# Performance work log

Measured on AMD Instinct MI355X. Metric: run time of the kernel, lower is better.

The kernel has to match this reference:

```python
import jax, jax.numpy as jnp
import numpy as np

NUM_HEADS = 8
KEY_DIM = 16
BLOCK = 8
HALO = 3
KV_K = BLOCK + 2 * HALO          # kv_kernel = 14
EMB = NUM_HEADS * KEY_DIM        # 128


def setup_inputs() -> dict:
    key = jax.random.key(0)
    ks = jax.random.split(key, 6)
    B, H, W, C = 8, 80, 80, 128
    std = KEY_DIM ** -0.5
    return {
        "inputs": jax.random.normal(ks[0], (B, H, W, C), jnp.float32),
        "query_dense": jax.random.normal(ks[1], (C, EMB), jnp.float32) * 0.05,
        "kv_dense": jax.random.normal(ks[2], (C, 2 * EMB), jnp.float32) * 0.05,
        "out_dense": jax.random.normal(ks[3], (EMB, C), jnp.float32) * 0.05,
        "pos_emb_w": jax.random.normal(ks[4], (KEY_DIM, 2 * KV_K - 1), jnp.float32) * std,
        "pos_emb_h": jax.random.normal(ks[5], (KEY_DIM, 2 * KV_K - 1), jnp.float32) * std,
    }


def rel_to_abs(rel_pos):
    # [b, heads, hh, ww, 2*pos_dim-1] -> [b, heads, hh, ww, pos_dim]
    b, heads, hh, ww, dim = rel_pos.shape
    pos_dim = (dim + 1) // 2
    gap = pos_dim - ww if ww > 1 else 2
    flat = rel_pos.reshape(b, heads, hh, ww * dim)
    flat = flat[:, :, :, ww - 1:-1] if ww > 1 else flat[:, :, :, 1:]
    out = flat.reshape(b, heads, hh, ww, 2 * (pos_dim - 1))
    return out[..., gap:pos_dim + gap]


def relative_logits(pos_q, pe_w, pe_h):
    # pos_q: [b, n, qb, qb, key_dim]
    rl_w = rel_to_abs(jnp.einsum('bnxyd,dk->bnxyk', pos_q, pe_w))                       # [b,n,qb,qb,KV_K]
    qh = pos_q.transpose(0, 1, 3, 2, 4)
    rl_h = rel_to_abs(jnp.einsum('bnxyd,dk->bnxyk', qh, pe_h)).transpose(0, 1, 3, 2, 4)  # [b,n,qb,qb,KV_K]
    return rl_w[..., None, :] + rl_h[..., :, None]                                       # [b,n,qb,qb,KV_K,KV_K]


def reference(inputs, query_dense, kv_dense, out_dense, pos_emb_w, pos_emb_h):
    B, H, W, C = inputs.shape
    scale = 1.0 / jnp.sqrt(jnp.asarray(KEY_DIM, inputs.dtype))
    query = jnp.einsum('bhwc,cd->bhwd', inputs, query_dense) * scale
    hq, wq = H // BLOCK, W // BLOCK
    q = query.reshape(B, hq, BLOCK, wq, BLOCK, NUM_HEADS, KEY_DIM).transpose(0, 5, 1, 3, 2, 4, 6)
    attn_q = q.reshape(B, NUM_HEADS, hq, wq, BLOCK * BLOCK, KEY_DIM)
    pos_q = q.reshape(B, NUM_HEADS * hq * wq, BLOCK, BLOCK, KEY_DIM)

    kv = jnp.einsum('bhwc,cd->bhwd', inputs, kv_dense)
    kvp = jnp.pad(kv, ((0, 0), (HALO, HALO), (HALO, HALO), (0, 0)))
    # overlapping halo windows: stride BLOCK, window KV_K (matches tf.image.extract_patches)
    ridx = jnp.arange(hq)[:, None] * BLOCK + jnp.arange(KV_K)[None, :]
    cidx = jnp.arange(wq)[:, None] * BLOCK + jnp.arange(KV_K)[None, :]
    patches = kvp[:, ridx][:, :, :, cidx]                 # [B,hq,KV,wq,KV,2*EMB]
    patches = patches.transpose(0, 1, 3, 2, 4, 5)         # [B,hq,wq,KV,KV,2*EMB]
    kv_inp = patches.reshape(B, hq, wq, KV_K, KV_K, NUM_HEADS, 2 * KEY_DIM)
    kv_inp = kv_inp.transpose(0, 5, 1, 2, 3, 4, 6).reshape(B, NUM_HEADS, hq, wq, KV_K * KV_K, 2 * KEY_DIM)
    k, v = kv_inp[..., :KEY_DIM], kv_inp[..., KEY_DIM:]

    scores = jnp.einsum('bnhwqd,bnhwkd->bnhwqk', attn_q, k)   # [B,heads,hq,wq,64,196]
    pos = relative_logits(pos_q, pos_emb_w, pos_emb_h)
    scores = scores + pos.reshape(scores.shape)
    attn = jax.nn.softmax(scores, axis=-1)
    out = jnp.einsum('bnhwqk,bnhwkd->bnhwqd', attn, v)
    out = out.reshape(B, NUM_HEADS, hq, wq, BLOCK, BLOCK, KEY_DIM)
    out = out.transpose(0, 2, 4, 3, 5, 1, 6).reshape(B, H, W, EMB)
    return jnp.einsum('bhwe,eo->bhwo', out, out_dense)
```

## Files before the change

### kernel.cpp

```cpp
#include <hip/hip_runtime.h>
#include <cstddef>

namespace {
constexpr int BATCH = 8;
constexpr int HDIM  = 80;
constexpr int WDIM  = 80;
constexpr int CDIM  = 128;
constexpr int NH    = 8;
constexpr int KD    = 16;
constexpr int BLK   = 8;
constexpr int HALO  = 3;
constexpr int KVK   = 14;
constexpr int EMB   = 128;
constexpr int HQ    = 10;
constexpr int WQ    = 10;
constexpr int MROWS = BATCH * HDIM * WDIM;
constexpr int QKV_N = 384;

constexpr int KPAD  = 24;
constexpr int M2PAD = 36;
constexpr int PEPAD = 20;
constexpr int APAD  = 136;
}

typedef _Float16 f16;
typedef f16   f16x2 __attribute__((ext_vector_type(2)));
typedef f16   f16x4 __attribute__((ext_vector_type(4)));
typedef f16   f16x8 __attribute__((ext_vector_type(8)));
typedef float f32x4 __attribute__((ext_vector_type(4)));

__global__ __launch_bounds__(256) void convert_weights(
    const float* __restrict__ qd, const float* __restrict__ kvd,
    const float* __restrict__ od, const float* __restrict__ pew,
    const float* __restrict__ peh,
    f16* __restrict__ BTqkv, f16* __restrict__ BTo, f16* __restrict__ peT)
{
  const float QSC = 0.25f * 1.4426950408889634f;
  int tid = blockIdx.x * 256 + threadIdx.x;
  if (tid < 384 * 128) {
    int n = tid >> 7, c = tid & 127;
    float v = (n < 128) ? qd[c * 128 + n] * QSC : kvd[c * 256 + (n - 128)];
    BTqkv[tid] = (f16)v;
  } else if (tid < 384 * 128 + 128 * 128) {
    int j = tid - 384 * 128;
    int o = j >> 7, e = j & 127;
    BTo[j] = (f16)od[e * 128 + o];
  } else {
    int j = tid - (384 * 128 + 128 * 128);
    int which = j / 640;
    int rem   = j - which * 640;
    int col   = rem / PEPAD;
    int d     = rem - col * PEPAD;
    float v = 0.f;
    if (col < 27 && d < 16) v = (which ? peh : pew)[d * 27 + col];
    peT[j] = (f16)v;
  }
}

__global__ __launch_bounds__(256, 4) void gemm_qkv_mfma(
    const float* __restrict__ A, const f16* __restrict__ BT,
    f16* __restrict__ C)
{
  __shared__ __align__(16) f16 b_lds[128 * APAD];

  const int bid = blockIdx.x;
  const int xcd = bid & 7;
  const int idx = bid >> 3;
  const int m0 = (xcd * 50 + idx / 3) * 128;
  const int n0 = (idx % 3) * 128;
  const int t  = threadIdx.x;

  #pragma unroll
  for (int it = 0; it < 8; ++it) {
    int item = t + it * 256;
    int row = item >> 4, c8 = item & 15;
    *reinterpret_cast<f16x8*>(&b_lds[row * APAD + c8 * 8]) =
        *reinterpret_cast<const f16x8*>(BT + (size_t)(n0 + row) * CDIM + c8 * 8);
  }
  __syncthreads();

  const int lane = t & 63, wv = t >> 6;
  const int g = lane >> 4, qi = lane & 15;

  const float* ap0 = A + (size_t)(m0 + wv * 32 + qi) * CDIM + g * 4;
  const float* ap1 = ap0 + 16 * CDIM;

  f32x4 acc[2][8];
  #pragma unroll
  for (int mt = 0; mt < 2; ++mt)
    #pragma unroll
    for (int nt = 0; nt < 8; ++nt) acc[mt][nt] = {0.f, 0.f, 0.f, 0.f};

  #pragma unroll
  for (int ks = 0; ks < 8; ++ks) {
    float4 fa0 = *reinterpret_cast<const float4*>(ap0 + ks * 16);
    float4 fa1 = *reinterpret_cast<const float4*>(ap1 + ks * 16);
    f16x4 a0 = {(f16)fa0.x, (f16)fa0.y, (f16)fa0.z, (f16)fa0.w};
    f16x4 a1 = {(f16)fa1.x, (f16)fa1.y, (f16)fa1.z, (f16)fa1.w};
    #pragma unroll
    for (int nt = 0; nt < 8; ++nt) {
      f16x4 bf = *reinterpret_cast<const f16x4*>(
          &b_lds[(nt * 16 + qi) * APAD + ks * 16 + g * 4]);
      acc[0][nt] = __builtin_amdgcn_mfma_f32_16x16x16f16(bf, a0, acc[0][nt], 0, 0, 0);
      acc[1][nt] = __builtin_amdgcn_mfma_f32_16x16x16f16(bf, a1, acc[1][nt], 0, 0, 0);
    }
  }

  #pragma unroll
  for (int mt = 0; mt < 2; ++mt) {
    int m = m0 + wv * 32 + mt * 16 + qi;
    #pragma unroll
    for (int nt = 0; nt < 8; ++nt) {
      f16x4 h = {(f16)acc[mt][nt][0], (f16)acc[mt][nt][1],
                 (f16)acc[mt][nt][2], (f16)acc[mt][nt][3]};
      *reinterpret_cast<f16x4*>(&C[(size_t)m * QKV_N + n0 + nt * 16 + g * 4]) = h;
    }
  }
}

__global__ __launch_bounds__(256, 4) void halo_attn_mfma(
    const f16* __restrict__ qkv, const f16* __restrict__ peT,
    f16* __restrict__ O)
{
  __shared__ __align__(16) f16 k_lds[224 * KPAD];
  __shared__ __align__(16) f16 v_lds[224 * 16];
  __shared__ __align__(16) f16 m2_lds[64 * M2PAD];

  const int d0w  = blockIdx.x;
  const int bid  = (d0w & 7) * 800 + (d0w >> 3);
  const int n    = bid & 7;
  const int tile = bid >> 3;
  const int tw   = tile % WQ;
  const int th   = (tile / WQ) % HQ;
  const int b    = tile / (WQ * HQ);
  const int t    = threadIdx.x;

  const int lane = t & 63;
  const int wv   = t >> 6;
  const int g    = lane >> 4;
  const int qi   = lane & 15;
  const int q0   = wv * 16;
  const int q    = q0 + qi;
  const int x    = q >> 3, y = q & 7;

  const size_t qrow = ((size_t)(b * HDIM + th * BLK + x)) * WDIM + tw * BLK + y;
  f16x4 qf = *reinterpret_cast<const f16x4*>(&qkv[qrow * QKV_N + n * KD + g * 4]);

  #pragma unroll
  for (int it = 0; it < 4; ++it) {
    int item = t + it * 256;
    if (item < 896) {
      int slot = item >> 2, part = item & 3;
      int kh = slot >> 4, kw = slot & 15;
      int hh = th * BLK - HALO + kh;
      int ww = tw * BLK - HALO + kw;
      f16x8 v = {};
      if ((unsigned)hh < (unsigned)HDIM && (unsigned)ww < (unsigned)WDIM) {
        size_t row = ((size_t)(b * HDIM + hh)) * WDIM + ww;
        v = *reinterpret_cast<const f16x8*>(
            &qkv[row * QKV_N + 128 + n * 32 + part * 8]);
      }
      if (part < 2)
        *reinterpret_cast<f16x8*>(&k_lds[slot * KPAD + part * 8]) = v;
      else
        *reinterpret_cast<f16x8*>(&v_lds[slot * 16 + (part - 2) * 8]) = v;
    }
  }

  const f32x4 z4 = {0.f, 0.f, 0.f, 0.f};

  #pragma unroll
  for (int which = 0; which < 2; ++which) {
    #pragma unroll
    for (int ct = 0; ct < 2; ++ct) {
      f16x4 pf = *reinterpret_cast<const f16x4*>(
          &peT[(which * 32 + ct * 16 + qi) * PEPAD + g * 4]);
      f32x4 mc = __builtin_amdgcn_mfma_f32_16x16x16f16(qf, pf, z4, 0, 0, 0);
      int colb = ct * 16 + qi;
      #pragma unroll
      for (int r = 0; r < 4; ++r) {
        int qr = q0 + g * 4 + r;
        if (which == 0) {
          int kw = colb - 13 + (qr & 7);
          if ((unsigned)kw < 16u) m2_lds[qr * M2PAD + kw] = (f16)mc[r];
        } else {
          int tt = colb - 13 + (qr >> 3);
          if ((unsigned)tt < 14u) m2_lds[qr * M2PAD + 16 + tt] = (f16)mc[r];
        }
      }
    }
  }

  f16x4 rlwv = *reinterpret_cast<const f16x4*>(&m2_lds[q * M2PAD + g * 4]);
  f16x4 rh4[4];
  #pragma unroll
  for (int k = 0; k < 4; ++k)
    rh4[k] = *reinterpret_cast<const f16x4*>(&m2_lds[q * M2PAD + 16 + k * 4]);

  float rlw[4];
  #pragma unroll
  for (int r = 0; r < 4; ++r) rlw[r] = (float)rlwv[r];
  if (g == 3) { rlw[2] = -1e30f; rlw[3] = -1e30f; }

  __syncthreads();

  f32x4 s[14];
  #pragma unroll
  for (int tt = 0; tt < 14; ++tt) {
    float rh = (float)rh4[tt >> 2][tt & 3];
    f32x4 c;
    c[0] = rlw[0] + rh; c[1] = rlw[1] + rh;
    c[2] = rlw[2] + rh; c[3] = rlw[3] + rh;
    f16x4 kf = *reinterpret_cast<const f16x4*>(&k_lds[(tt * 16 + qi) * KPAD + g * 4]);
    s[tt] = __builtin_amdgcn_mfma_f32_16x16x16f16(kf, qf, c, 0, 0, 0);
  }

  float ls = 0.f;
  f16x4 pf[14];
  #pragma unroll
  for (int tt = 0; tt < 14; ++tt) {
    float p0 = __builtin_amdgcn_exp2f(s[tt][0]);
    float p1 = __builtin_amdgcn_exp2f(s[tt][1]);
    float p2 = __builtin_amdgcn_exp2f(s[tt][2]);
    float p3 = __builtin_amdgcn_exp2f(s[tt][3]);
    ls += (p0 + p1) + (p2 + p3);
    f16x2 lo = __builtin_bit_cast(f16x2, __builtin_amdgcn_cvt_pkrtz(p0, p1));
    f16x2 hi = __builtin_bit_cast(f16x2, __builtin_amdgcn_cvt_pkrtz(p2, p3));
    pf[tt][0] = lo[0]; pf[tt][1] = lo[1];
    pf[tt][2] = hi[0]; pf[tt][3] = hi[1];
  }
  ls += __shfl_xor(ls, 16);
  ls += __shfl_xor(ls, 32);

  f16x4 iv;
  #pragma unroll
  for (int r = 0; r < 4; ++r)
    iv[r] = (qi == g * 4 + r) ? (f16)1.f : (f16)0.f;

  f32x4 acc = z4;
  #pragma unroll
  for (int tt = 0; tt < 14; ++tt) {
    f16x4 xv = *reinterpret_cast<const f16x4*>(&v_lds[(tt * 16 + qi) * 16 + g * 4]);
    f32x4 tD = __builtin_amdgcn_mfma_f32_16x16x16f16(xv, iv, z4, 0, 0, 0);
    f16x2 lo = __builtin_bit_cast(f16x2, __builtin_amdgcn_cvt_pkrtz(tD[0], tD[1]));
    f16x2 hi = __builtin_bit_cast(f16x2, __builtin_amdgcn_cvt_pkrtz(tD[2], tD[3]));
    f16x4 vf;
    vf[0] = lo[0]; vf[1] = lo[1]; vf[2] = hi[0]; vf[3] = hi[1];
    acc = __builtin_amdgcn_mfma_f32_16x16x16f16(vf, pf[tt], acc, 0, 0, 0);
  }

  const float inv = __builtin_amdgcn_rcpf(ls);
  f16x4 o = {(f16)(acc[0] * inv), (f16)(acc[1] * inv),
             (f16)(acc[2] * inv), (f16)(acc[3] * inv)};
  *reinterpret_cast<f16x4*>(&O[qrow * EMB + n * KD + g * 4]) = o;
}

__global__ __launch_bounds__(256, 4) void gemm_out_mfma(
    const f16* __restrict__ A, const f16* __restrict__ BT,
    float* __restrict__ C)
{
  __shared__ __align__(16) f16 b_lds[128 * APAD];

  const int m0 = blockIdx.x * 64;
  const int t  = threadIdx.x;

  #pragma unroll
  for (int it = 0; it < 8; ++it) {
    int item = t + it * 256;
    int row = item >> 4, c8 = item & 15;
    *reinterpret_cast<f16x8*>(&b_lds[row * APAD + c8 * 8]) =
        *reinterpret_cast<const f16x8*>(BT + (size_t)row * EMB + c8 * 8);
  }
  __syncthreads();

  const int lane = t & 63, wv = t >> 6;
  const int g = lane >> 4, qi = lane & 15;

  const f16* ap = A + (size_t)(m0 + wv * 16 + qi) * EMB + g * 4;

  f32x4 acc[8];
  #pragma unroll
  for (int nt = 0; nt < 8; ++nt) acc[nt] = {0.f, 0.f, 0.f, 0.f};

  #pragma unroll
  for (int ks = 0; ks < 8; ++ks) {
    f16x4 a = *reinterpret_cast<const f16x4*>(ap + ks * 16);
    #pragma unroll
    for (int nt = 0; nt < 8; ++nt) {
      f16x4 bf = *reinterpret_cast<const f16x4*>(
          &b_lds[(nt * 16 + qi) * APAD + ks * 16 + g * 4]);
      acc[nt] = __builtin_amdgcn_mfma_f32_16x16x16f16(bf, a, acc[nt], 0, 0, 0);
    }
  }

  const int m = m0 + wv * 16 + qi;
  #pragma unroll
  for (int nt = 0; nt < 8; ++nt) {
    f32x4 v = acc[nt];
    *reinterpret_cast<float4*>(&C[(size_t)m * CDIM + nt * 16 + g * 4]) =
        *reinterpret_cast<float4*>(&v);
  }
}

extern "C" void kernel_launch(void* const* d_in, const int* in_sizes, int n_in,
                              void* d_out, int out_size, void* d_ws, size_t ws_size,
                              hipStream_t stream)
{
  const float* inputs = (const float*)d_in[0];
  const float* qd     = (const float*)d_in[1];
  const float* kvd    = (const float*)d_in[2];
  const float* od     = (const float*)d_in[3];
  const float* pew    = (const float*)d_in[4];
  const float* peh    = (const float*)d_in[5];

  char* ws = (char*)d_ws;
  f16* qkv   = (f16*)ws;
  f16* O     = (f16*)(ws + (size_t)MROWS * QKV_N * 2);
  f16* BTqkv = (f16*)(ws + (size_t)MROWS * QKV_N * 2 + (size_t)MROWS * EMB * 2);
  f16* BTo   = BTqkv + 384 * 128;
  f16* peT   = BTo + 128 * 128;
  float* out = (float*)d_out;

  convert_weights<<<dim3(261), 256, 0, stream>>>(qd, kvd, od, pew, peh,
                                                 BTqkv, BTo, peT);
  gemm_qkv_mfma<<<dim3(1200), 256, 0, stream>>>(inputs, BTqkv, qkv);
  halo_attn_mfma<<<dim3(BATCH * HQ * WQ * NH), 256, 0, stream>>>(qkv, peT, O);
  gemm_out_mfma<<<dim3(MROWS / 64), 256, 0, stream>>>(O, BTo, out);
}
```

Baseline: 73.25 us.

## Store K/V in per-head zero-padded spatial layout for branch-free halo loads

The QKV GEMM now writes Q to its own buffer and scatters K/V into a per-(batch, head) spatially padded buffer (86x88x32). A new kernel zeroes the 3-pixel halo border. The attention kernel then loads halo windows without bounds checks, and each head's 64-byte K/V row sits contiguously with its neighbours. In exchange there is an extra small launch, and the GEMM epilogue does more scattered stores with index math.

```diff
diff --git a/kernel.cpp b/kernel.cpp
--- a/kernel.cpp
+++ b/kernel.cpp
@@ -16,6 +16,11 @@
 constexpr int WQ    = 10;
 constexpr int MROWS = BATCH * HDIM * WDIM;
 constexpr int QKV_N = 384;
+
+constexpr int PH    = 86;
+constexpr int PW    = 88;
+constexpr int KVCH  = 32;
+constexpr int HEADSZ = PH * PW * KVCH;
 
 constexpr int KPAD  = 24;
 constexpr int M2PAD = 36;
@@ -57,9 +62,28 @@
   }
 }
 
+__global__ __launch_bounds__(256) void zero_pad(f16* __restrict__ kvp)
+{
+  f16* base = kvp + (size_t)blockIdx.x * HEADSZ;
+  for (int item = threadIdx.x; item < 1168 * 4; item += 256) {
+    int cell = item >> 2, part = item & 3;
+    int hh, ww;
+    if (cell < 6 * PW) {
+      int r = cell / PW; ww = cell - r * PW;
+      hh = (r < 3) ? r : 80 + r;
+    } else {
+      int c = cell - 6 * PW;
+      int r = c >> 3, cc = c & 7;
+      hh = 3 + r;
+      ww = (cc < 3) ? cc : 80 + cc;
+    }
+    *reinterpret_cast<f16x8*>(base + (hh * PW + ww) * KVCH + part * 8) = f16x8{};
+  }
+}
+
 __global__ __launch_bounds__(256, 4) void gemm_qkv_mfma(
     const float* __restrict__ A, const f16* __restrict__ BT,
-    f16* __restrict__ C)
+    f16* __restrict__ Qbuf, f16* __restrict__ kvp)
 {
   __shared__ __align__(16) f16 b_lds[128 * APAD];
 
@@ -109,18 +133,34 @@
   #pragma unroll
   for (int mt = 0; mt < 2; ++mt) {
     int m = m0 + wv * 32 + mt * 16 + qi;
-    #pragma unroll
-    for (int nt = 0; nt < 8; ++nt) {
-      f16x4 h = {(f16)acc[mt][nt][0], (f16)acc[mt][nt][1],
-                 (f16)acc[mt][nt][2], (f16)acc[mt][nt][3]};
-      *reinterpret_cast<f16x4*>(&C[(size_t)m * QKV_N + n0 + nt * 16 + g * 4]) = h;
+    if (n0 == 0) {
+      #pragma unroll
+      for (int nt = 0; nt < 8; ++nt) {
+        f16x4 h = {(f16)acc[mt][nt][0], (f16)acc[mt][nt][1],
+                   (f16)acc[mt][nt][2], (f16)acc[mt][nt][3]};
+        *reinterpret_cast<f16x4*>(&Qbuf[(size_t)m * EMB + nt * 16 + g * 4]) = h;
+      }
+    } else {
+      int bb  = m / 6400;
+      int rem = m - bb * 6400;
+      int hh  = rem / 80;
+      int ww  = rem - hh * 80;
+      size_t pbase = (size_t)bb * (NH * HEADSZ) + ((hh + 3) * PW + (ww + 3)) * KVCH;
+      #pragma unroll
+      for (int nt = 0; nt < 8; ++nt) {
+        int col  = (n0 - 128) + nt * 16 + g * 4;
+        int head = col >> 5, cc = col & 31;
+        f16x4 h = {(f16)acc[mt][nt][0], (f16)acc[mt][nt][1],
+                   (f16)acc[mt][nt][2], (f16)acc[mt][nt][3]};
+        *reinterpret_cast<f16x4*>(&kvp[pbase + (size_t)head * HEADSZ + cc]) = h;
+      }
     }
   }
 }
 
 __global__ __launch_bounds__(256, 4) void halo_attn_mfma(
-    const f16* __restrict__ qkv, const f16* __restrict__ peT,
-    f16* __restrict__ O)
+    const f16* __restrict__ Qbuf, const f16* __restrict__ kvp,
+    const f16* __restrict__ peT, f16* __restrict__ O)
 {
   __shared__ __align__(16) f16 k_lds[224 * KPAD];
   __shared__ __align__(16) f16 v_lds[224 * 16];
@@ -144,22 +184,18 @@
   const int x    = q >> 3, y = q & 7;
 
   const size_t qrow = ((size_t)(b * HDIM + th * BLK + x)) * WDIM + tw * BLK + y;
-  f16x4 qf = *reinterpret_cast<const f16x4*>(&qkv[qrow * QKV_N + n * KD + g * 4]);
-
+  f16x4 qf = *reinterpret_cast<const f16x4*>(&Qbuf[qrow * EMB + n * KD + g * 4]);
+
+  const f16* kvbase = kvp + (size_t)(b * NH + n) * HEADSZ
+                    + ((th * BLK) * PW + tw * BLK) * KVCH;
   #pragma unroll
   for (int it = 0; it < 4; ++it) {
     int item = t + it * 256;
     if (item < 896) {
       int slot = item >> 2, part = item & 3;
       int kh = slot >> 4, kw = slot & 15;
-      int hh = th * BLK - HALO + kh;
-      int ww = tw * BLK - HALO + kw;
-      f16x8 v = {};
-      if ((unsigned)hh < (unsigned)HDIM && (unsigned)ww < (unsigned)WDIM) {
-        size_t row = ((size_t)(b * HDIM + hh)) * WDIM + ww;
-        v = *reinterpret_cast<const f16x8*>(
-            &qkv[row * QKV_N + 128 + n * 32 + part * 8]);
-      }
+      f16x8 v = *reinterpret_cast<const f16x8*>(
+          kvbase + kh * (PW * KVCH) + kw * KVCH + part * 8);
       if (part < 2)
         *reinterpret_cast<f16x8*>(&k_lds[slot * KPAD + part * 8]) = v;
       else
@@ -313,17 +349,18 @@
   const float* pew    = (const float*)d_in[4];
   const float* peh    = (const float*)d_in[5];
 
-  char* ws = (char*)d_ws;
-  f16* qkv   = (f16*)ws;
-  f16* O     = (f16*)(ws + (size_t)MROWS * QKV_N * 2);
-  f16* BTqkv = (f16*)(ws + (size_t)MROWS * QKV_N * 2 + (size_t)MROWS * EMB * 2);
+  f16* Qbuf  = (f16*)d_ws;
+  f16* kvp   = Qbuf + (size_t)MROWS * EMB;
+  f16* O     = kvp + (size_t)BATCH * NH * HEADSZ;
+  f16* BTqkv = O + (size_t)MROWS * EMB;
   f16* BTo   = BTqkv + 384 * 128;
   f16* peT   = BTo + 128 * 128;
   float* out = (float*)d_out;
 
   convert_weights<<<dim3(261), 256, 0, stream>>>(qd, kvd, od, pew, peh,
                                                  BTqkv, BTo, peT);
-  gemm_qkv_mfma<<<dim3(1200), 256, 0, stream>>>(inputs, BTqkv, qkv);
-  halo_attn_mfma<<<dim3(BATCH * HQ * WQ * NH), 256, 0, stream>>>(qkv, peT, O);
+  zero_pad<<<dim3(BATCH * NH), 256, 0, stream>>>(kvp);
+  gemm_qkv_mfma<<<dim3(1200), 256, 0, stream>>>(inputs, BTqkv, Qbuf, kvp);
+  halo_attn_mfma<<<dim3(BATCH * HQ * WQ * NH), 256, 0, stream>>>(Qbuf, kvp, peT, O);
   gemm_out_mfma<<<dim3(MROWS / 64), 256, 0, stream>>>(O, BTo, out);
 }
```

Result: no change. 74.63 us (+1.9%).

## Fuse output projection into halo attention kernel, looping heads per block

Applied to the files above, without the earlier changes.

The attention kernel now processes all 8 heads of a spatial tile inside one block, accumulating each head's output times the matching slice of the output projection into per-thread fp32 accumulators. It then writes the final fp32 output directly, which removes the separate output GEMM launch and the f16 intermediate O buffer round trip. In exchange the grid shrinks from 6400 to 800 blocks, each running a serial head loop with extra barriers. The projection weights are read from global memory instead of LDS, and launch bounds drop to 3 blocks per SM to make room for the added accumulator registers.

```diff
diff --git a/kernel.cpp b/kernel.cpp
--- a/kernel.cpp
+++ b/kernel.cpp
@@ -118,21 +118,19 @@
   }
 }
 
-__global__ __launch_bounds__(256, 4) void halo_attn_mfma(
+__global__ __launch_bounds__(256, 3) void halo_attn_fused(
     const f16* __restrict__ qkv, const f16* __restrict__ peT,
-    f16* __restrict__ O)
+    const f16* __restrict__ BTo, float* __restrict__ out)
 {
   __shared__ __align__(16) f16 k_lds[224 * KPAD];
   __shared__ __align__(16) f16 v_lds[224 * 16];
   __shared__ __align__(16) f16 m2_lds[64 * M2PAD];
 
   const int d0w  = blockIdx.x;
-  const int bid  = (d0w & 7) * 800 + (d0w >> 3);
-  const int n    = bid & 7;
-  const int tile = bid >> 3;
-  const int tw   = tile % WQ;
-  const int th   = (tile / WQ) % HQ;
-  const int b    = tile / (WQ * HQ);
+  const int bid  = (d0w & 7) * 100 + (d0w >> 3);
+  const int tw   = bid % WQ;
+  const int th   = (bid / WQ) % HQ;
+  const int b    = bid / (WQ * HQ);
   const int t    = threadIdx.x;
 
   const int lane = t & 63;
@@ -144,160 +142,134 @@
   const int x    = q >> 3, y = q & 7;
 
   const size_t qrow = ((size_t)(b * HDIM + th * BLK + x)) * WDIM + tw * BLK + y;
-  f16x4 qf = *reinterpret_cast<const f16x4*>(&qkv[qrow * QKV_N + n * KD + g * 4]);
-
-  #pragma unroll
-  for (int it = 0; it < 4; ++it) {
-    int item = t + it * 256;
-    if (item < 896) {
-      int slot = item >> 2, part = item & 3;
-      int kh = slot >> 4, kw = slot & 15;
-      int hh = th * BLK - HALO + kh;
-      int ww = tw * BLK - HALO + kw;
-      f16x8 v = {};
-      if ((unsigned)hh < (unsigned)HDIM && (unsigned)ww < (unsigned)WDIM) {
-        size_t row = ((size_t)(b * HDIM + hh)) * WDIM + ww;
-        v = *reinterpret_cast<const f16x8*>(
-            &qkv[row * QKV_N + 128 + n * 32 + part * 8]);
+  const f32x4 z4 = {0.f, 0.f, 0.f, 0.f};
+
+  f32x4 out_acc[8];
+  #pragma unroll
+  for (int nt = 0; nt < 8; ++nt) out_acc[nt] = z4;
+
+  for (int n = 0; n < NH; ++n) {
+    __syncthreads();
+
+    f16x4 qf = *reinterpret_cast<const f16x4*>(&qkv[qrow * QKV_N + n * KD + g * 4]);
+
+    #pragma unroll
+    for (int it = 0; it < 4; ++it) {
+      int item = t + it * 256;
+      if (item < 896) {
+        int slot = item >> 2, part = item & 3;
+        int kh = slot >> 4, kw = slot & 15;
+        int hh = th * BLK - HALO + kh;
+        int ww = tw * BLK - HALO + kw;
+        f16x8 v = {};
+        if ((unsigned)hh < (unsigned)HDIM && (unsigned)ww < (unsigned)WDIM) {
+          size_t row = ((size_t)(b * HDIM + hh)) * WDIM + ww;
+          v = *reinterpret_cast<const f16x8*>(
+              &qkv[row * QKV_N + 128 + n * 32 + part * 8]);
+        }
+        if (part < 2)
+          *reinterpret_cast<f16x8*>(&k_lds[slot * KPAD + part * 8]) = v;
+        else
+          *reinterpret_cast<f16x8*>(&v_lds[slot * 16 + (part - 2) * 8]) = v;
       }
-      if (part < 2)
-        *reinterpret_cast<f16x8*>(&k_lds[slot * KPAD + part * 8]) = v;
-      else
-        *reinterpret_cast<f16x8*>(&v_lds[slot * 16 + (part - 2) * 8]) = v;
-    }
-  }
-
-  const f32x4 z4 = {0.f, 0.f, 0.f, 0.f};
-
-  #pragma unroll
-  for (int which = 0; which < 2; ++which) {
-    #pragma unroll
-    for (int ct = 0; ct < 2; ++ct) {
-      f16x4 pf = *reinterpret_cast<const f16x4*>(
-          &peT[(which * 32 + ct * 16 + qi) * PEPAD + g * 4]);
-      f32x4 mc = __builtin_amdgcn_mfma_f32_16x16x16f16(qf, pf, z4, 0, 0, 0);
-      int colb = ct * 16 + qi;
+    }
+
+    #pragma unroll
+    for (int which = 0; which < 2; ++which) {
       #pragma unroll
-      for (int r = 0; r < 4; ++r) {
-        int qr = q0 + g * 4 + r;
-        if (which == 0) {
-          int kw = colb - 13 + (qr & 7);
-          if ((unsigned)kw < 16u) m2_lds[qr * M2PAD + kw] = (f16)mc[r];
-        } else {
-          int tt = colb - 13 + (qr >> 3);
-          if ((unsigned)tt < 14u) m2_lds[qr * M2PAD + 16 + tt] = (f16)mc[r];
+      for (int ct = 0; ct < 2; ++ct) {
+        f16x4 pf = *reinterpret_cast<const f16x4*>(
+            &peT[(which * 32 + ct * 16 + qi) * PEPAD + g * 4]);
+        f32x4 mc = __builtin_amdgcn_mfma_f32_16x16x16f16(qf, pf, z4, 0, 0, 0);
+        int colb = ct * 16 + qi;
+        #pragma unroll
+        for (int r = 0; r < 4; ++r) {
+          int qr = q0 + g * 4 + r;
+          if (which == 0) {
+            int kw = colb - 13 + (qr & 7);
+            if ((unsigned)kw < 16u) m2_lds[qr * M2PAD + kw] = (f16)mc[r];
+          } else {
+            int tt = colb - 13 + (qr >> 3);
+            if ((unsigned)tt < 14u) m2_lds[qr * M2PAD + 16 + tt] = (f16)mc[r];
+          }
         }
       }
     }
-  }
-
-  f16x4 rlwv = *reinterpret_cast<const f16x4*>(&m2_lds[q * M2PAD + g * 4]);
-  f16x4 rh4[4];
-  #pragma unroll
-  for (int k = 0; k < 4; ++k)
-    rh4[k] = *reinterpret_cast<const f16x4*>(&m2_lds[q * M2PAD + 16 + k * 4]);
-
-  float rlw[4];
-  #pragma unroll
-  for (int r = 0; r < 4; ++r) rlw[r] = (float)rlwv[r];
-  if (g == 3) { rlw[2] = -1e30f; rlw[3] = -1e30f; }
-
-  __syncthreads();
-
-  f32x4 s[14];
-  #pragma unroll
-  for (int tt = 0; tt < 14; ++tt) {
-    float rh = (float)rh4[tt >> 2][tt & 3];
-    f32x4 c;
-    c[0] = rlw[0] + rh; c[1] = rlw[1] + rh;
-    c[2] = rlw[2] + rh; c[3] = rlw[3] + rh;
-    f16x4 kf = *reinterpret_cast<const f16x4*>(&k_lds[(tt * 16 + qi) * KPAD + g * 4]);
-    s[tt] = __builtin_amdgcn_mfma_f32_16x16x16f16(kf, qf, c, 0, 0, 0);
-  }
-
-  float ls = 0.f;
-  f16x4 pf[14];
-  #pragma unroll
-  for (int tt = 0; tt < 14; ++tt) {
-    float p0 = __builtin_amdgcn_exp2f(s[tt][0]);
-    float p1 = __builtin_amdgcn_exp2f(s[tt][1]);
-    float p2 = __builtin_amdgcn_exp2f(s[tt][2]);
-    float p3 = __builtin_amdgcn_exp2f(s[tt][3]);
-    ls += (p0 + p1) + (p2 + p3);
-    f16x2 lo = __builtin_bit_cast(f16x2, __builtin_amdgcn_cvt_pkrtz(p0, p1));
-    f16x2 hi = __builtin_bit_cast(f16x2, __builtin_amdgcn_cvt_pkrtz(p2, p3));
-    pf[tt][0] = lo[0]; pf[tt][1] = lo[1];
-    pf[tt][2] = hi[0]; pf[tt][3] = hi[1];
-  }
-  ls += __shfl_xor(ls, 16);
-  ls += __shfl_xor(ls, 32);
-
-  f16x4 iv;
-  #pragma unroll
-  for (int r = 0; r < 4; ++r)
-    iv[r] = (qi == g * 4 + r) ? (f16)1.f : (f16)0.f;
-
-  f32x4 acc = z4;
-  #pragma unroll
-  for (int tt = 0; tt < 14; ++tt) {
-    f16x4 xv = *reinterpret_cast<const f16x4*>(&v_lds[(tt * 16 + qi) * 16 + g * 4]);
-    f32x4 tD = __builtin_amdgcn_mfma_f32_16x16x16f16(xv, iv, z4, 0, 0, 0);
-    f16x2 lo = __builtin_bit_cast(f16x2, __builtin_amdgcn_cvt_pkrtz(tD[0], tD[1]));
-    f16x2 hi = __builtin_bit_cast(f16x2, __builtin_amdgcn_cvt_pkrtz(tD[2], tD[3]));
-    f16x4 vf;
-    vf[0] = lo[0]; vf[1] = lo[1]; vf[2] = hi[0]; vf[3] = hi[1];
-    acc = __builtin_amdgcn_mfma_f32_16x16x16f16(vf, pf[tt], acc, 0, 0, 0);
-  }
-
-  const float inv = __builtin_amdgcn_rcpf(ls);
-  f16x4 o = {(f16)(acc[0] * inv), (f16)(acc[1] * inv),
-             (f16)(acc[2] * inv), (f16)(acc[3] * inv)};
-  *reinterpret_cast<f16x4*>(&O[qrow * EMB + n * KD + g * 4]) = o;
-}
-
-__global__ __launch_bounds__(256, 4) void gemm_out_mfma(
-    const f16* __restrict__ A, const f16* __restrict__ BT,
-    float* __restrict__ C)
-{
-  __shared__ __align__(16) f16 b_lds[128 * APAD];
-
-  const int m0 = blockIdx.x * 64;
-  const int t  = threadIdx.x;
-
-  #pragma unroll
-  for (int it = 0; it < 8; ++it) {
-    int item = t + it * 256;
-    int row = item >> 4, c8 = item & 15;
-    *reinterpret_cast<f16x8*>(&b_lds[row * APAD + c8 * 8]) =
-        *reinterpret_cast<const f16x8*>(BT + (size_t)row * EMB + c8 * 8);
-  }
-  __syncthreads();
-
-  const int lane = t & 63, wv = t >> 6;
-  const int g = lane >> 4, qi = lane & 15;
-
-  const f16* ap = A + (size_t)(m0 + wv * 16 + qi) * EMB + g * 4;
-
-  f32x4 acc[8];
-  #pragma unroll
-  for (int nt = 0; nt < 8; ++nt) acc[nt] = {0.f, 0.f, 0.f, 0.f};
-
-  #pragma unroll
-  for (int ks = 0; ks < 8; ++ks) {
-    f16x4 a = *reinterpret_cast<const f16x4*>(ap + ks * 16);
+
+    f16x4 rlwv = *reinterpret_cast<const f16x4*>(&m2_lds[q * M2PAD + g * 4]);
+    f16x4 rh4[4];
+    #pragma unroll
+    for (int k = 0; k < 4; ++k)
+      rh4[k] = *reinterpret_cast<const f16x4*>(&m2_lds[q * M2PAD + 16 + k * 4]);
+
+    float rlw[4];
+    #pragma unroll
+    for (int r = 0; r < 4; ++r) rlw[r] = (float)rlwv[r];
+    if (g == 3) { rlw[2] = -1e30f; rlw[3] = -1e30f; }
+
+    __syncthreads();
+
+    f32x4 s[14];
+    #pragma unroll
+    for (int tt = 0; tt < 14; ++tt) {
+      float rh = (float)rh4[tt >> 2][tt & 3];
+      f32x4 c;
+      c[0] = rlw[0] + rh; c[1] = rlw[1] + rh;
+      c[2] = rlw[2] + rh; c[3] = rlw[3] + rh;
+      f16x4 kf = *reinterpret_cast<const f16x4*>(&k_lds[(tt * 16 + qi) * KPAD + g * 4]);
+      s[tt] = __builtin_amdgcn_mfma_f32_16x16x16f16(kf, qf, c, 0, 0, 0);
+    }
+
+    float ls = 0.f;
+    f16x4 pf[14];
+    #pragma unroll
+    for (int tt = 0; tt < 14; ++tt) {
+      float p0 = __builtin_amdgcn_exp2f(s[tt][0]);
+      float p1 = __builtin_amdgcn_exp2f(s[tt][1]);
+      float p2 = __builtin_amdgcn_exp2f(s[tt][2]);
+      float p3 = __builtin_amdgcn_exp2f(s[tt][3]);
+      ls += (p0 + p1) + (p2 + p3);
+      f16x2 lo = __builtin_bit_cast(f16x2, __builtin_amdgcn_cvt_pkrtz(p0, p1));
+      f16x2 hi = __builtin_bit_cast(f16x2, __builtin_amdgcn_cvt_pkrtz(p2, p3));
+      pf[tt][0] = lo[0]; pf[tt][1] = lo[1];
+      pf[tt][2] = hi[0]; pf[tt][3] = hi[1];
+    }
+    ls += __shfl_xor(ls, 16);
+    ls += __shfl_xor(ls, 32);
+
+    f16x4 iv;
+    #pragma unroll
+    for (int r = 0; r < 4; ++r)
+      iv[r] = (qi == g * 4 + r) ? (f16)1.f : (f16)0.f;
+
+    f32x4 acc = z4;
+    #pragma unroll
+    for (int tt = 0; tt < 14; ++tt) {
+      f16x4 xv = *reinterpret_cast<const f16x4*>(&v_lds[(tt * 16 + qi) * 16 + g * 4]);
+      f32x4 tD = __builtin_amdgcn_mfma_f32_16x16x16f16(xv, iv, z4, 0, 0, 0);
+      f16x2 lo = __builtin_bit_cast(f16x2, __builtin_amdgcn_cvt_pkrtz(tD[0], tD[1]));
+      f16x2 hi = __builtin_bit_cast(f16x2, __builtin_amdgcn_cvt_pkrtz(tD[2], tD[3]));
+      f16x4 vf;
+      vf[0] = lo[0]; vf[1] = lo[1]; vf[2] = hi[0]; vf[3] = hi[1];
+      acc = __builtin_amdgcn_mfma_f32_16x16x16f16(vf, pf[tt], acc, 0, 0, 0);
+    }
+
+    const float inv = __builtin_amdgcn_rcpf(ls);
+    f16x4 of = {(f16)(acc[0] * inv), (f16)(acc[1] * inv),
+                (f16)(acc[2] * inv), (f16)(acc[3] * inv)};
+
     #pragma unroll
     for (int nt = 0; nt < 8; ++nt) {
       f16x4 bf = *reinterpret_cast<const f16x4*>(
-          &b_lds[(nt * 16 + qi) * APAD + ks * 16 + g * 4]);
-      acc[nt] = __builtin_amdgcn_mfma_f32_16x16x16f16(bf, a, acc[nt], 0, 0, 0);
-    }
-  }
-
-  const int m = m0 + wv * 16 + qi;
+          &BTo[(size_t)(nt * 16 + qi) * EMB + n * KD + g * 4]);
+      out_acc[nt] = __builtin_amdgcn_mfma_f32_16x16x16f16(bf, of, out_acc[nt], 0, 0, 0);
+    }
+  }
+
   #pragma unroll
   for (int nt = 0; nt < 8; ++nt) {
-    f32x4 v = acc[nt];
-    *reinterpret_cast<float4*>(&C[(size_t)m * CDIM + nt * 16 + g * 4]) =
+    f32x4 v = out_acc[nt];
+    *reinterpret_cast<float4*>(&out[qrow * EMB + nt * 16 + g * 4]) =
         *reinterpret_cast<float4*>(&v);
   }
 }
@@ -315,8 +287,7 @@
 
   char* ws = (char*)d_ws;
   f16* qkv   = (f16*)ws;
-  f16* O     = (f16*)(ws + (size_t)MROWS * QKV_N * 2);
-  f16* BTqkv = (f16*)(ws + (size_t)MROWS * QKV_N * 2 + (size_t)MROWS * EMB * 2);
+  f16* BTqkv = (f16*)(ws + (size_t)MROWS * QKV_N * 2);
   f16* BTo   = BTqkv + 384 * 128;
   f16* peT   = BTo + 128 * 128;
   float* out = (float*)d_out;
@@ -324,6 +295,5 @@
   convert_weights<<<dim3(261), 256, 0, stream>>>(qd, kvd, od, pew, peh,
                                                  BTqkv, BTo, peT);
   gemm_qkv_mfma<<<dim3(1200), 256, 0, stream>>>(inputs, BTqkv, qkv);
-  halo_attn_mfma<<<dim3(BATCH * HQ * WQ * NH), 256, 0, stream>>>(qkv, peT, O);
-  gemm_out_mfma<<<dim3(MROWS / 64), 256, 0, stream>>>(O, BTo, out);
-}
+  halo_attn_fused<<<dim3(BATCH * HQ * WQ), 256, 0, stream>>>(qkv, peT, BTo, out);
+}
```

Result: slower. 101.8 us (+38.9%).
